# Kernel optimization log

Hardware: AMD Instinct MI355X
Metric: run time of the kernel (lower is better)

The kernel has to match this reference:

```python
import jax, jax.numpy as jnp
import numpy as np

N_NODES = 50000
N_EDGES = 1600000
D_FEAT = 512
FILTERS = 256
NUM_CLASSES = 16


def setup_inputs() -> dict:
    key = jax.random.key(0)
    k = jax.random.split(key, 6)
    x = jax.random.normal(k[0], (N_NODES, D_FEAT), dtype=jnp.float32)
    W1 = jax.random.normal(k[1], (D_FEAT, FILTERS), dtype=jnp.float32) * (1.0 / np.sqrt(D_FEAT))
    W2 = jax.random.normal(k[2], (FILTERS, NUM_CLASSES), dtype=jnp.float32) * (1.0 / np.sqrt(FILTERS))
    edge_weight = jax.random.uniform(k[3], (N_EDGES,), dtype=jnp.float32)
    edge_src = jax.random.randint(k[4], (N_EDGES,), 0, N_NODES, dtype=jnp.int32)
    edge_dst = jax.random.randint(k[5], (N_EDGES,), 0, N_NODES, dtype=jnp.int32)
    return {"x": x, "W1": W1, "W2": W2, "edge_weight": edge_weight,
            "edge_src": edge_src, "edge_dst": edge_dst}


def _propagate(h, edge_src, edge_dst, edge_weight):
    # sparse A @ h: out[dst] += w * h[src]
    msgs = edge_weight[:, None] * h[edge_src]          # [E, F]
    return jax.ops.segment_sum(msgs, edge_dst, num_segments=N_NODES)


def reference(x, W1, W2, edge_weight, edge_src, edge_dst):
    # Dropout layers are identity at inference (training=False).
    # Layer 1: relu(A @ (X @ W1))
    h = jax.nn.relu(_propagate(x @ W1, edge_src, edge_dst, edge_weight))
    # Layer 2: softmax(A @ (H @ W2))
    logits = _propagate(h @ W2, edge_src, edge_dst, edge_weight)
    return jax.nn.softmax(logits, axis=-1)
```

## Files before the change

kernel.cpp:

```cpp
#include <hip/hip_runtime.h>

#define N_NODES 50000
#define N_EDGES 1600000
#define D_FEAT 512
#define FILTERS 256
#define NUM_CLASSES 16

typedef __bf16 bf16x8 __attribute__((ext_vector_type(8)));
typedef float f32x4 __attribute__((ext_vector_type(4)));
typedef _Float16 half4 __attribute__((ext_vector_type(4)));
typedef _Float16 f16x8 __attribute__((ext_vector_type(8)));

#define GLOAD_LDS16(g, l)                                                  \
  __builtin_amdgcn_global_load_lds(                                        \
      (const __attribute__((address_space(1))) unsigned int*)(g),          \
      (__attribute__((address_space(3))) unsigned int*)(l), 16, 0, 0)

__global__ __launch_bounds__(256) void split_w1_kernel(
    const float* __restrict__ W1, __bf16* __restrict__ Wth,
    __bf16* __restrict__ Wtl) {
  const int idx = blockIdx.x * 256 + threadIdx.x;
  const int k = idx >> 8;
  const int n = idx & 255;
  const float v = W1[idx];
  const __bf16 h = (__bf16)v;
  const __bf16 l = (__bf16)(v - (float)h);
  Wth[n * D_FEAT + k] = h;
  Wtl[n * D_FEAT + k] = l;
}

__global__ __launch_bounds__(256) void gemm1_mfma_kernel(
    const float* __restrict__ A, const __bf16* __restrict__ Bh,
    const __bf16* __restrict__ Bl, _Float16* __restrict__ C) {
  const int K = D_FEAT;
  __shared__ __bf16 sAh[128 * 32];
  __shared__ __bf16 sAl[128 * 32];
  __shared__ __bf16 sBh[128 * 32];
  __shared__ __bf16 sBl[128 * 32];

  const int tid = threadIdx.x;
  const int wave = tid >> 6;
  const int lane = tid & 63;
  const int wm = (wave >> 1) * 64;
  const int wn = (wave & 1) * 64;
  const int m0 = blockIdx.x * 128;
  const int n0 = blockIdx.y * 128;

  const int arow = tid >> 1;
  const int aks = (tid & 1) * 16;
  int am = m0 + arow;
  if (am >= N_NODES) am = N_NODES - 1;
  const float* aptr = A + (size_t)am * K + aks;

  const int lr = lane >> 2;
  const int lc = (lane & 3) * 8;
  const int fm = lane & 15;
  const int fq = lane >> 4;

  f32x4 acc[4][4] = {};

  for (int k0 = 0; k0 < K; k0 += 32) {
    const float4* ap = (const float4*)(aptr + k0);
    const float4 a0 = ap[0], a1 = ap[1], a2 = ap[2], a3 = ap[3];

    __syncthreads();

#pragma unroll
    for (int i = 0; i < 2; ++i) {
      const int row = wave * 32 + i * 16;
      GLOAD_LDS16(Bh + (size_t)(n0 + row + lr) * K + k0 + lc, sBh + row * 32);
      GLOAD_LDS16(Bl + (size_t)(n0 + row + lr) * K + k0 + lc, sBl + row * 32);
    }

    float va[16] = {a0.x, a0.y, a0.z, a0.w, a1.x, a1.y, a1.z, a1.w,
                    a2.x, a2.y, a2.z, a2.w, a3.x, a3.y, a3.z, a3.w};
    __bf16 hh[16], ll[16];
#pragma unroll
    for (int i = 0; i < 16; ++i) {
      const __bf16 h = (__bf16)va[i];
      hh[i] = h;
      ll[i] = (__bf16)(va[i] - (float)h);
    }
    *(bf16x8*)(sAh + arow * 32 + aks) = *(bf16x8*)&hh[0];
    *(bf16x8*)(sAh + arow * 32 + aks + 8) = *(bf16x8*)&hh[8];
    *(bf16x8*)(sAl + arow * 32 + aks) = *(bf16x8*)&ll[0];
    *(bf16x8*)(sAl + arow * 32 + aks + 8) = *(bf16x8*)&ll[8];

    __syncthreads();

    bf16x8 fah[4], fal[4], fbh[4], fbl[4];
#pragma unroll
    for (int t = 0; t < 4; ++t) {
      const int moff = (wm + t * 16 + fm) * 32 + fq * 8;
      fah[t] = *(const bf16x8*)(sAh + moff);
      fal[t] = *(const bf16x8*)(sAl + moff);
      const int noff = (wn + t * 16 + fm) * 32 + fq * 8;
      fbh[t] = *(const bf16x8*)(sBh + noff);
      fbl[t] = *(const bf16x8*)(sBl + noff);
    }
#pragma unroll
    for (int i = 0; i < 4; ++i)
#pragma unroll
      for (int j = 0; j < 4; ++j)
        acc[i][j] = __builtin_amdgcn_mfma_f32_16x16x32_bf16(fah[i], fbh[j],
                                                            acc[i][j], 0, 0, 0);
#pragma unroll
    for (int i = 0; i < 4; ++i)
#pragma unroll
      for (int j = 0; j < 4; ++j)
        acc[i][j] = __builtin_amdgcn_mfma_f32_16x16x32_bf16(fah[i], fbl[j],
                                                            acc[i][j], 0, 0, 0);
#pragma unroll
    for (int i = 0; i < 4; ++i)
#pragma unroll
      for (int j = 0; j < 4; ++j)
        acc[i][j] = __builtin_amdgcn_mfma_f32_16x16x32_bf16(fal[i], fbh[j],
                                                            acc[i][j], 0, 0, 0);
  }

#pragma unroll
  for (int ti = 0; ti < 4; ++ti) {
#pragma unroll
    for (int r = 0; r < 4; ++r) {
      const int m = m0 + wm + ti * 16 + fq * 4 + r;
      if (m < N_NODES) {
#pragma unroll
        for (int tj = 0; tj < 4; ++tj) {
          const int n = n0 + wn + tj * 16 + fm;
          C[(size_t)m * FILTERS + n] = (_Float16)acc[ti][tj][r];
        }
      }
    }
  }
}

__global__ __launch_bounds__(256) void hist_kernel(const int* __restrict__ edst,
                                                   int* __restrict__ deg) {
  const int e = blockIdx.x * 256 + threadIdx.x;
  if (e < N_EDGES) atomicAdd(&deg[edst[e]], 1);
}

#define SCAN_NB 196
__global__ __launch_bounds__(256) void scan_blocks_kernel(
    const int* __restrict__ deg, int* __restrict__ row_ptr,
    int* __restrict__ bsum) {
  __shared__ int s[256];
  const int i = blockIdx.x * 256 + threadIdx.x;
  const int v = (i < N_NODES) ? deg[i] : 0;
  s[threadIdx.x] = v;
  __syncthreads();
  for (int off = 1; off < 256; off <<= 1) {
    const int t = (threadIdx.x >= off) ? s[threadIdx.x - off] : 0;
    __syncthreads();
    s[threadIdx.x] += t;
    __syncthreads();
  }
  if (i < N_NODES) row_ptr[i] = s[threadIdx.x] - v;
  if (threadIdx.x == 255) bsum[blockIdx.x] = s[255];
}

__global__ __launch_bounds__(256) void scan_sums_kernel(int* __restrict__ bsum) {
  __shared__ int s[256];
  const int v = (threadIdx.x < SCAN_NB) ? bsum[threadIdx.x] : 0;
  s[threadIdx.x] = v;
  __syncthreads();
  for (int off = 1; off < 256; off <<= 1) {
    const int t = (threadIdx.x >= off) ? s[threadIdx.x - off] : 0;
    __syncthreads();
    s[threadIdx.x] += t;
    __syncthreads();
  }
  if (threadIdx.x < SCAN_NB) bsum[threadIdx.x] = s[threadIdx.x] - v;
}

__global__ __launch_bounds__(256) void scan_add_kernel(
    int* __restrict__ row_ptr, const int* __restrict__ bsum,
    int* __restrict__ cursor) {
  const int i = blockIdx.x * 256 + threadIdx.x;
  if (i < N_NODES) {
    const int r = row_ptr[i] + bsum[blockIdx.x];
    row_ptr[i] = r;
    cursor[i] = r;
  }
  if (i == 0) row_ptr[N_NODES] = N_EDGES;
}

__global__ __launch_bounds__(256) void fill_kernel(
    const int* __restrict__ esrc, const int* __restrict__ edst,
    const float* __restrict__ ew, int* __restrict__ cursor,
    int4* __restrict__ meta) {
  const int e = blockIdx.x * 256 + threadIdx.x;
  if (e >= N_EDGES) return;
  const int d = edst[e];
  const int pos = atomicAdd(&cursor[d], 1);
  meta[pos] = make_int4(esrc[e], __float_as_int(ew[e]), d, 0);
}

__global__ __launch_bounds__(256) void gather1_gemm2_kernel(
    const _Float16* __restrict__ xw1, const int* __restrict__ row_ptr,
    const int4* __restrict__ meta, const float* __restrict__ W2,
    _Float16* __restrict__ h2) {
  __shared__ float red[4][16][17];
  const int wave = threadIdx.x >> 6;
  const int lane = threadIdx.x & 63;
  const int node = blockIdx.x * 4 + wave;
  const int beg = row_ptr[node];
  const int end = row_ptr[node + 1];

  float acc[4] = {};
  const half4* __restrict__ xw1v = (const half4*)xw1;

  for (int c0 = beg; c0 < end; c0 += 64) {
    const int cnt = min(64, end - c0);
    const int4 mv = meta[c0 + ((lane < cnt) ? lane : 0)];

    for (int j = 0; j < cnt; j += 8) {
      int srcs[8];
      float ws[8];
#pragma unroll
      for (int u = 0; u < 8; ++u) {
        const int live = (j + u < cnt);
        const int l = live ? (j + u) : 0;
        srcs[u] = __builtin_amdgcn_readlane(mv.x, l);
        const int wb = __builtin_amdgcn_readlane(mv.y, l);
        ws[u] = live ? __int_as_float(wb) : 0.f;
      }
      half4 v[8];
#pragma unroll
      for (int u = 0; u < 8; ++u)
        v[u] = xw1v[(unsigned)srcs[u] * 64u + (unsigned)lane];
#pragma unroll
      for (int u = 0; u < 8; ++u)
#pragma unroll
        for (int i = 0; i < 4; ++i)
          acc[i] = fmaf(ws[u], (float)v[u][i], acc[i]);
    }
  }

  float r[4];
#pragma unroll
  for (int i = 0; i < 4; ++i) r[i] = fmaxf(acc[i], 0.f);

  float p[16] = {};
#pragma unroll
  for (int j = 0; j < 4; ++j) {
    const float4* wr = (const float4*)(W2 + (size_t)(lane * 4 + j) * NUM_CLASSES);
#pragma unroll
    for (int c4 = 0; c4 < 4; ++c4) {
      const float4 wv = wr[c4];
      p[c4 * 4 + 0] = fmaf(r[j], wv.x, p[c4 * 4 + 0]);
      p[c4 * 4 + 1] = fmaf(r[j], wv.y, p[c4 * 4 + 1]);
      p[c4 * 4 + 2] = fmaf(r[j], wv.z, p[c4 * 4 + 2]);
      p[c4 * 4 + 3] = fmaf(r[j], wv.w, p[c4 * 4 + 3]);
    }
  }

#pragma unroll
  for (int off = 32; off >= 16; off >>= 1)
#pragma unroll
    for (int i = 0; i < 16; ++i) p[i] += __shfl_xor(p[i], off, 64);

  if (lane < 16) {
#pragma unroll
    for (int i = 0; i < 16; ++i) red[wave][lane][i] = p[i];
  }
  if (lane < 16) {
    float sum = 0.f;
#pragma unroll
    for (int i = 0; i < 16; ++i) sum += red[wave][i][lane];
    h2[(size_t)node * NUM_CLASSES + lane] = (_Float16)sum;
  }
}

__global__ __launch_bounds__(256) void gather2_mfma_kernel(
    const _Float16* __restrict__ h2, const int* __restrict__ row_ptr,
    const int4* __restrict__ meta, float* __restrict__ out) {
  __shared__ _Float16 lds[4][16][72];
  const int wave = threadIdx.x >> 6;
  const int lane = threadIdx.x & 63;
  const int tile = blockIdx.x * 4 + wave;
  if (tile >= N_NODES / 16) return;
  const int t0 = tile * 16;
  const int beg = row_ptr[t0];
  const int end = row_ptr[t0 + 16];

  const int cls = lane & 15;
  const int kq = lane >> 4;
  const int erow = lane >> 1;
  const int part = lane & 1;

  f32x4 acc = {0.f, 0.f, 0.f, 0.f};
  _Float16* myl = &lds[wave][0][0];

  if (beg < end) {
    const int last = end - 1;
    int e = beg + lane;
    int4 m = meta[(e <= last) ? e : last];
    float wv = (e <= last) ? __int_as_float(m.y) : 0.f;

    for (int c0 = beg; c0 < end; c0 += 64) {
      int4 mn = m;
      float wn = 0.f;
      const int c1 = c0 + 64;
      if (c1 < end) {
        const int en = c1 + lane;
        mn = meta[(en <= last) ? en : last];
        wn = (en <= last) ? __int_as_float(mn.y) : 0.f;
      }

      const int se0 = __shfl(m.x, erow, 64);
      const int se1 = __shfl(m.x, 32 + erow, 64);
      const f16x8 r0 =
          *(const f16x8*)(h2 + (size_t)se0 * NUM_CLASSES + part * 8);
      const f16x8 r1 =
          *(const f16x8*)(h2 + (size_t)se1 * NUM_CLASSES + part * 8);

      f16x8 a0, a1;
#pragma unroll
      for (int j = 0; j < 8; ++j) {
        const int ei = kq * 8 + j;
        const int d0 = __shfl(m.z, ei, 64) - t0;
        const float w0 = __shfl(wv, ei, 64);
        a0[j] = (d0 == cls) ? (_Float16)w0 : (_Float16)0.f;
        const int d1 = __shfl(m.z, 32 + ei, 64) - t0;
        const float w1 = __shfl(wv, 32 + ei, 64);
        a1[j] = (d1 == cls) ? (_Float16)w1 : (_Float16)0.f;
      }

#pragma unroll
      for (int j = 0; j < 8; ++j) myl[(part * 8 + j) * 72 + erow] = r0[j];
#pragma unroll
      for (int j = 0; j < 8; ++j) myl[(part * 8 + j) * 72 + 32 + erow] = r1[j];

      const f16x8 b0 = *(const f16x8*)(myl + cls * 72 + kq * 8);
      const f16x8 b1 = *(const f16x8*)(myl + cls * 72 + 32 + kq * 8);

      acc = __builtin_amdgcn_mfma_f32_16x16x32_f16(a0, b0, acc, 0, 0, 0);
      acc = __builtin_amdgcn_mfma_f32_16x16x32_f16(a1, b1, acc, 0, 0, 0);

      m = mn;
      wv = wn;
    }
  }

#pragma unroll
  for (int r = 0; r < 4; ++r) {
    const float a = acc[r];
    float mx = a;
#pragma unroll
    for (int off = 8; off >= 1; off >>= 1)
      mx = fmaxf(mx, __shfl_xor(mx, off, 16));
    const float ex = __expf(a - mx);
    float sm = ex;
#pragma unroll
    for (int off = 8; off >= 1; off >>= 1) sm += __shfl_xor(sm, off, 16);
    out[(size_t)(t0 + kq * 4 + r) * NUM_CLASSES + cls] = ex / sm;
  }
}

extern "C" void kernel_launch(void* const* d_in, const int* in_sizes, int n_in,
                              void* d_out, int out_size, void* d_ws,
                              size_t ws_size, hipStream_t stream) {
  const float* x = (const float*)d_in[0];
  const float* W1 = (const float*)d_in[1];
  const float* W2 = (const float*)d_in[2];
  const float* ew = (const float*)d_in[3];
  const int* esrc = (const int*)d_in[4];
  const int* edst = (const int*)d_in[5];
  float* out = (float*)d_out;

  _Float16* xw1 = (_Float16*)d_ws;
  _Float16* h2 = xw1 + (size_t)N_NODES * FILTERS;
  int* row_ptr = (int*)(h2 + (size_t)N_NODES * NUM_CLASSES);
  int* cursor = row_ptr + (N_NODES + 1);
  int* deg = cursor + N_NODES;
  int4* meta = (int4*)(((uintptr_t)(deg + N_NODES) + 15) & ~(uintptr_t)15);
  __bf16* w1th = (__bf16*)(meta + N_EDGES);
  __bf16* w1tl = w1th + D_FEAT * FILTERS;
  int* bsum = (int*)(w1tl + D_FEAT * FILTERS);

  hipMemsetAsync(deg, 0, N_NODES * sizeof(int), stream);
  hist_kernel<<<(N_EDGES + 255) / 256, 256, 0, stream>>>(edst, deg);
  scan_blocks_kernel<<<SCAN_NB, 256, 0, stream>>>(deg, row_ptr, bsum);
  scan_sums_kernel<<<1, 256, 0, stream>>>(bsum);
  scan_add_kernel<<<SCAN_NB, 256, 0, stream>>>(row_ptr, bsum, cursor);
  fill_kernel<<<(N_EDGES + 255) / 256, 256, 0, stream>>>(esrc, edst, ew,
                                                         cursor, meta);

  split_w1_kernel<<<(D_FEAT * FILTERS) / 256, 256, 0, stream>>>(W1, w1th, w1tl);
  dim3 g1((N_NODES + 127) / 128, FILTERS / 128);
  gemm1_mfma_kernel<<<g1, 256, 0, stream>>>(x, w1th, w1tl, xw1);

  gather1_gemm2_kernel<<<N_NODES / 4, 256, 0, stream>>>(xw1, row_ptr, meta, W2,
                                                        h2);

  gather2_mfma_kernel<<<(N_NODES / 16 + 3) / 4, 256, 0, stream>>>(h2, row_ptr,
                                                                  meta, out);
}
```

Before: 564.1 us.

## Gather two edges per wave with 16-byte loads and software-pipelined issue

```diff
diff --git a/kernel.cpp b/kernel.cpp
--- a/kernel.cpp
+++ b/kernel.cpp
@@ -207,44 +207,68 @@
   const int beg = row_ptr[node];
   const int end = row_ptr[node + 1];
 
-  float acc[4] = {};
-  const half4* __restrict__ xw1v = (const half4*)xw1;
+  const int eh = lane >> 5;
+  const int oct = lane & 31;
+
+  float acc[8] = {};
+
+#define G1_ISSUE(V, W, JB)                                                 \
+  {                                                                        \
+    _Pragma("unroll") for (int u = 0; u < 8; ++u) {                        \
+      const int e0 = (JB) + 2 * u;                                         \
+      const int e1 = e0 + 1;                                               \
+      const int l0 = (e0 < cnt) ? e0 : 0;                                  \
+      const int l1 = (e1 < cnt) ? e1 : 0;                                  \
+      const int s0 = __builtin_amdgcn_readlane(mv.x, l0);                  \
+      const int s1 = __builtin_amdgcn_readlane(mv.x, l1);                  \
+      const int q0 = __builtin_amdgcn_readlane(mv.y, l0);                  \
+      const int q1 = __builtin_amdgcn_readlane(mv.y, l1);                  \
+      const float w0f = (e0 < cnt) ? __int_as_float(q0) : 0.f;             \
+      const float w1f = (e1 < cnt) ? __int_as_float(q1) : 0.f;             \
+      W[u] = eh ? w1f : w0f;                                               \
+      const unsigned rs = eh ? (unsigned)s1 : (unsigned)s0;                \
+      V[u] = *(const f16x8*)(xw1 + (size_t)rs * FILTERS + oct * 8);        \
+    }                                                                      \
+  }
+
+#define G1_CONSUME(V, W)                                                   \
+  {                                                                        \
+    _Pragma("unroll") for (int u = 0; u < 8; ++u)                          \
+        _Pragma("unroll") for (int i = 0; i < 8; ++i) acc[i] =             \
+        fmaf(W[u], (float)V[u][i], acc[i]);                                \
+  }
 
   for (int c0 = beg; c0 < end; c0 += 64) {
     const int cnt = min(64, end - c0);
     const int4 mv = meta[c0 + ((lane < cnt) ? lane : 0)];
-
-    for (int j = 0; j < cnt; j += 8) {
-      int srcs[8];
-      float ws[8];
-#pragma unroll
-      for (int u = 0; u < 8; ++u) {
-        const int live = (j + u < cnt);
-        const int l = live ? (j + u) : 0;
-        srcs[u] = __builtin_amdgcn_readlane(mv.x, l);
-        const int wb = __builtin_amdgcn_readlane(mv.y, l);
-        ws[u] = live ? __int_as_float(wb) : 0.f;
+    const int ng = (cnt + 15) >> 4;
+
+    f16x8 va[8], vb[8];
+    float wa[8], wb[8];
+    G1_ISSUE(va, wa, 0);
+    for (int g = 1; g < ng; g += 2) {
+      G1_ISSUE(vb, wb, g * 16);
+      G1_CONSUME(va, wa);
+      if (g + 1 < ng) {
+        G1_ISSUE(va, wa, (g + 1) * 16);
       }
-      half4 v[8];
-#pragma unroll
-      for (int u = 0; u < 8; ++u)
-        v[u] = xw1v[(unsigned)srcs[u] * 64u + (unsigned)lane];
-#pragma unroll
-      for (int u = 0; u < 8; ++u)
-#pragma unroll
-        for (int i = 0; i < 4; ++i)
-          acc[i] = fmaf(ws[u], (float)v[u][i], acc[i]);
-    }
-  }
+      G1_CONSUME(vb, wb);
+    }
+    if (ng & 1) G1_CONSUME(va, wa);
+  }
+
+#pragma unroll
+  for (int i = 0; i < 8; ++i) acc[i] += __shfl_xor(acc[i], 32, 64);
 
   float r[4];
 #pragma unroll
-  for (int i = 0; i < 4; ++i) r[i] = fmaxf(acc[i], 0.f);
+  for (int j = 0; j < 4; ++j) r[j] = fmaxf(acc[eh * 4 + j], 0.f);
 
   float p[16] = {};
 #pragma unroll
   for (int j = 0; j < 4; ++j) {
-    const float4* wr = (const float4*)(W2 + (size_t)(lane * 4 + j) * NUM_CLASSES);
+    const float4* wr =
+        (const float4*)(W2 + (size_t)(oct * 8 + eh * 4 + j) * NUM_CLASSES);
 #pragma unroll
     for (int c4 = 0; c4 < 4; ++c4) {
       const float4 wv = wr[c4];
```

Result: slower. 577.6 us (+2.4%).

## Chunk XW1 by 32-feature slabs and split layer-1 gather across chunks

Applied to the files above, without the earlier changes.

```diff
diff --git a/kernel.cpp b/kernel.cpp
--- a/kernel.cpp
+++ b/kernel.cpp
@@ -127,7 +127,8 @@
 #pragma unroll
         for (int tj = 0; tj < 4; ++tj) {
           const int n = n0 + wn + tj * 16 + fm;
-          C[(size_t)m * FILTERS + n] = (_Float16)acc[ti][tj][r];
+          C[(size_t)(n >> 5) * ((size_t)N_NODES * 32) + (size_t)m * 32 +
+            (n & 31)] = (_Float16)acc[ti][tj][r];
         }
       }
     }
@@ -196,80 +197,93 @@
   meta[pos] = make_int4(esrc[e], __float_as_int(ew[e]), d, 0);
 }
 
-__global__ __launch_bounds__(256) void gather1_gemm2_kernel(
-    const _Float16* __restrict__ xw1, const int* __restrict__ row_ptr,
-    const int4* __restrict__ meta, const float* __restrict__ W2,
-    _Float16* __restrict__ h2) {
-  __shared__ float red[4][16][17];
+__global__ __launch_bounds__(256) void pack_kernel(
+    const int4* __restrict__ meta, unsigned short* __restrict__ srcs,
+    float* __restrict__ ws) {
+  const int e = blockIdx.x * 256 + threadIdx.x;
+  if (e >= N_EDGES) return;
+  const int4 m = meta[e];
+  srcs[e] = (unsigned short)m.x;
+  ws[e] = __int_as_float(m.y);
+}
+
+__global__ __launch_bounds__(256) void gather1_chunk_kernel(
+    const _Float16* __restrict__ xw1c, const int* __restrict__ row_ptr,
+    const unsigned short* __restrict__ srcs, const float* __restrict__ ws,
+    const float* __restrict__ W2, float* __restrict__ h2acc) {
   const int wave = threadIdx.x >> 6;
   const int lane = threadIdx.x & 63;
-  const int node = blockIdx.x * 4 + wave;
+  const int chunk = blockIdx.x & 7;
+  const int node = (blockIdx.x >> 3) * 4 + wave;
+  const int g = lane >> 3;
+  const int il = lane & 7;
+  const _Float16* __restrict__ base =
+      xw1c + (size_t)chunk * ((size_t)N_NODES * 32) + il * 4;
+
+  float w2r[4][2];
+#pragma unroll
+  for (int j = 0; j < 4; ++j) {
+    const float2 t = *(const float2*)(W2 +
+        (size_t)(chunk * 32 + il * 4 + j) * NUM_CLASSES + g * 2);
+    w2r[j][0] = t.x;
+    w2r[j][1] = t.y;
+  }
+
   const int beg = row_ptr[node];
   const int end = row_ptr[node + 1];
-
   float acc[4] = {};
-  const half4* __restrict__ xw1v = (const half4*)xw1;
 
   for (int c0 = beg; c0 < end; c0 += 64) {
     const int cnt = min(64, end - c0);
-    const int4 mv = meta[c0 + ((lane < cnt) ? lane : 0)];
-
-    for (int j = 0; j < cnt; j += 8) {
-      int srcs[8];
-      float ws[8];
-#pragma unroll
-      for (int u = 0; u < 8; ++u) {
-        const int live = (j + u < cnt);
-        const int l = live ? (j + u) : 0;
-        srcs[u] = __builtin_amdgcn_readlane(mv.x, l);
-        const int wb = __builtin_amdgcn_readlane(mv.y, l);
-        ws[u] = live ? __int_as_float(wb) : 0.f;
-      }
-      half4 v[8];
-#pragma unroll
-      for (int u = 0; u < 8; ++u)
-        v[u] = xw1v[(unsigned)srcs[u] * 64u + (unsigned)lane];
-#pragma unroll
-      for (int u = 0; u < 8; ++u)
-#pragma unroll
-        for (int i = 0; i < 4; ++i)
-          acc[i] = fmaf(ws[u], (float)v[u][i], acc[i]);
-    }
-  }
-
-  float r[4];
-#pragma unroll
-  for (int i = 0; i < 4; ++i) r[i] = fmaxf(acc[i], 0.f);
-
-  float p[16] = {};
+    const int idx = c0 + ((lane < cnt) ? lane : 0);
+    const int sv = (int)srcs[idx];
+    const float wv = ws[idx];
+    const int npk = (cnt + 7) >> 3;
+    for (int p = 0; p < npk; p += 2) {
+      const int e0 = p * 8 + g;
+      const int e1 = e0 + 8;
+      const int s0 = __shfl(sv, e0, 64);
+      const int s1 = __shfl(sv, e1, 64);
+      float w0 = __shfl(wv, e0, 64);
+      float w1 = __shfl(wv, e1, 64);
+      w0 = (e0 < cnt) ? w0 : 0.f;
+      w1 = (e1 < cnt) ? w1 : 0.f;
+      const half4 v0 = *(const half4*)(base + (size_t)s0 * 32);
+      const half4 v1 = *(const half4*)(base + (size_t)s1 * 32);
+#pragma unroll
+      for (int i = 0; i < 4; ++i) acc[i] = fmaf(w0, (float)v0[i], acc[i]);
+#pragma unroll
+      for (int i = 0; i < 4; ++i) acc[i] = fmaf(w1, (float)v1[i], acc[i]);
+    }
+  }
+
+#pragma unroll
+  for (int off = 8; off <= 32; off <<= 1)
+#pragma unroll
+    for (int i = 0; i < 4; ++i) acc[i] += __shfl_xor(acc[i], off, 64);
+
+  float p0 = 0.f, p1 = 0.f;
 #pragma unroll
   for (int j = 0; j < 4; ++j) {
-    const float4* wr = (const float4*)(W2 + (size_t)(lane * 4 + j) * NUM_CLASSES);
-#pragma unroll
-    for (int c4 = 0; c4 < 4; ++c4) {
-      const float4 wv = wr[c4];
-      p[c4 * 4 + 0] = fmaf(r[j], wv.x, p[c4 * 4 + 0]);
-      p[c4 * 4 + 1] = fmaf(r[j], wv.y, p[c4 * 4 + 1]);
-      p[c4 * 4 + 2] = fmaf(r[j], wv.z, p[c4 * 4 + 2]);
-      p[c4 * 4 + 3] = fmaf(r[j], wv.w, p[c4 * 4 + 3]);
-    }
-  }
-
-#pragma unroll
-  for (int off = 32; off >= 16; off >>= 1)
-#pragma unroll
-    for (int i = 0; i < 16; ++i) p[i] += __shfl_xor(p[i], off, 64);
-
-  if (lane < 16) {
-#pragma unroll
-    for (int i = 0; i < 16; ++i) red[wave][lane][i] = p[i];
-  }
-  if (lane < 16) {
-    float sum = 0.f;
-#pragma unroll
-    for (int i = 0; i < 16; ++i) sum += red[wave][i][lane];
-    h2[(size_t)node * NUM_CLASSES + lane] = (_Float16)sum;
-  }
+    const float r = fmaxf(acc[j], 0.f);
+    p0 = fmaf(r, w2r[j][0], p0);
+    p1 = fmaf(r, w2r[j][1], p1);
+  }
+#pragma unroll
+  for (int off = 1; off <= 4; off <<= 1) {
+    p0 += __shfl_xor(p0, off, 64);
+    p1 += __shfl_xor(p1, off, 64);
+  }
+  if (il == 0) {
+    atomicAdd(&h2acc[(size_t)node * NUM_CLASSES + g * 2 + 0], p0);
+    atomicAdd(&h2acc[(size_t)node * NUM_CLASSES + g * 2 + 1], p1);
+  }
+}
+
+__global__ __launch_bounds__(256) void cvt_h2_kernel(
+    const float* __restrict__ a, _Float16* __restrict__ o) {
+  const int i = blockIdx.x * 256 + threadIdx.x;
+  o[i] = (_Float16)a[i];
 }
 
 __global__ __launch_bounds__(256) void gather2_mfma_kernel(
@@ -369,8 +383,8 @@
   const int* edst = (const int*)d_in[5];
   float* out = (float*)d_out;
 
-  _Float16* xw1 = (_Float16*)d_ws;
-  _Float16* h2 = xw1 + (size_t)N_NODES * FILTERS;
+  _Float16* xw1c = (_Float16*)d_ws;
+  _Float16* h2 = xw1c + (size_t)N_NODES * FILTERS;
   int* row_ptr = (int*)(h2 + (size_t)N_NODES * NUM_CLASSES);
   int* cursor = row_ptr + (N_NODES + 1);
   int* deg = cursor + N_NODES;
@@ -378,21 +392,28 @@
   __bf16* w1th = (__bf16*)(meta + N_EDGES);
   __bf16* w1tl = w1th + D_FEAT * FILTERS;
   int* bsum = (int*)(w1tl + D_FEAT * FILTERS);
+  float* h2acc = (float*)(bsum + 256);
+  unsigned short* srcs = (unsigned short*)(h2acc + (size_t)N_NODES * NUM_CLASSES);
+  float* ws = (float*)(srcs + N_EDGES);
 
   hipMemsetAsync(deg, 0, N_NODES * sizeof(int), stream);
+  hipMemsetAsync(h2acc, 0, (size_t)N_NODES * NUM_CLASSES * sizeof(float),
+                 stream);
   hist_kernel<<<(N_EDGES + 255) / 256, 256, 0, stream>>>(edst, deg);
   scan_blocks_kernel<<<SCAN_NB, 256, 0, stream>>>(deg, row_ptr, bsum);
   scan_sums_kernel<<<1, 256, 0, stream>>>(bsum);
   scan_add_kernel<<<SCAN_NB, 256, 0, stream>>>(row_ptr, bsum, cursor);
   fill_kernel<<<(N_EDGES + 255) / 256, 256, 0, stream>>>(esrc, edst, ew,
                                                          cursor, meta);
+  pack_kernel<<<(N_EDGES + 255) / 256, 256, 0, stream>>>(meta, srcs, ws);
 
   split_w1_kernel<<<(D_FEAT * FILTERS) / 256, 256, 0, stream>>>(W1, w1th, w1tl);
   dim3 g1((N_NODES + 127) / 128, FILTERS / 128);
-  gemm1_mfma_kernel<<<g1, 256, 0, stream>>>(x, w1th, w1tl, xw1);
-
-  gather1_gemm2_kernel<<<N_NODES / 4, 256, 0, stream>>>(xw1, row_ptr, meta, W2,
-                                                        h2);
+  gemm1_mfma_kernel<<<g1, 256, 0, stream>>>(x, w1th, w1tl, xw1c);
+
+  gather1_chunk_kernel<<<(N_NODES / 4) * 8, 256, 0, stream>>>(
+      xw1c, row_ptr, srcs, ws, W2, h2acc);
+  cvt_h2_kernel<<<(N_NODES * NUM_CLASSES) / 256, 256, 0, stream>>>(h2acc, h2);
 
   gather2_mfma_kernel<<<(N_NODES / 16 + 3) / 4, 256, 0, stream>>>(h2, row_ptr,
                                                                   meta, out);
```

After: 708.0 us. +25.5%, slower.

## Fuse CSR build and W1 split into one cooperative kernel with grid syncs

Applied to the files above, without the earlier changes.

```diff
diff --git a/kernel.cpp b/kernel.cpp
--- a/kernel.cpp
+++ b/kernel.cpp
@@ -1,4 +1,5 @@
 #include <hip/hip_runtime.h>
+#include <hip/hip_cooperative_groups.h>
 
 #define N_NODES 50000
 #define N_EDGES 1600000
@@ -16,17 +17,73 @@
       (const __attribute__((address_space(1))) unsigned int*)(g),          \
       (__attribute__((address_space(3))) unsigned int*)(l), 16, 0, 0)
 
-__global__ __launch_bounds__(256) void split_w1_kernel(
+#define CSR_NB 196
+__global__ __launch_bounds__(256) void csr_coop_kernel(
     const float* __restrict__ W1, __bf16* __restrict__ Wth,
-    __bf16* __restrict__ Wtl) {
-  const int idx = blockIdx.x * 256 + threadIdx.x;
-  const int k = idx >> 8;
-  const int n = idx & 255;
-  const float v = W1[idx];
-  const __bf16 h = (__bf16)v;
-  const __bf16 l = (__bf16)(v - (float)h);
-  Wth[n * D_FEAT + k] = h;
-  Wtl[n * D_FEAT + k] = l;
+    __bf16* __restrict__ Wtl, const int* __restrict__ esrc,
+    const int* __restrict__ edst, const float* __restrict__ ew,
+    int* __restrict__ deg, int* __restrict__ row_ptr,
+    int* __restrict__ cursor, int* __restrict__ bsum,
+    int4* __restrict__ meta) {
+  cooperative_groups::grid_group grid = cooperative_groups::this_grid();
+  const int tid = blockIdx.x * 256 + threadIdx.x;
+  const int nthr = CSR_NB * 256;
+
+  for (int i = tid; i < N_NODES; i += nthr) deg[i] = 0;
+  for (int i = tid; i < D_FEAT * FILTERS; i += nthr) {
+    const float v = W1[i];
+    const int k = i >> 8;
+    const int n = i & 255;
+    const __bf16 h = (__bf16)v;
+    Wth[n * D_FEAT + k] = h;
+    Wtl[n * D_FEAT + k] = (__bf16)(v - (float)h);
+  }
+  grid.sync();
+
+  for (int e = tid; e < N_EDGES; e += nthr) atomicAdd(&deg[edst[e]], 1);
+  grid.sync();
+
+  __shared__ int s[256];
+  const int v = (tid < N_NODES) ? deg[tid] : 0;
+  s[threadIdx.x] = v;
+  __syncthreads();
+  for (int off = 1; off < 256; off <<= 1) {
+    const int t = (threadIdx.x >= off) ? s[threadIdx.x - off] : 0;
+    __syncthreads();
+    s[threadIdx.x] += t;
+    __syncthreads();
+  }
+  const int excl = s[threadIdx.x] - v;
+  if (threadIdx.x == 255) bsum[blockIdx.x] = s[255];
+  grid.sync();
+
+  if (blockIdx.x == 0) {
+    const int bv = (threadIdx.x < CSR_NB) ? bsum[threadIdx.x] : 0;
+    s[threadIdx.x] = bv;
+    __syncthreads();
+    for (int off = 1; off < 256; off <<= 1) {
+      const int t = (threadIdx.x >= off) ? s[threadIdx.x - off] : 0;
+      __syncthreads();
+      s[threadIdx.x] += t;
+      __syncthreads();
+    }
+    if (threadIdx.x < CSR_NB) bsum[threadIdx.x] = s[threadIdx.x] - bv;
+  }
+  grid.sync();
+
+  if (tid < N_NODES) {
+    const int r = excl + bsum[blockIdx.x];
+    row_ptr[tid] = r;
+    cursor[tid] = r;
+  }
+  if (tid == 0) row_ptr[N_NODES] = N_EDGES;
+  grid.sync();
+
+  for (int e = tid; e < N_EDGES; e += nthr) {
+    const int d = edst[e];
+    const int pos = atomicAdd(&cursor[d], 1);
+    meta[pos] = make_int4(esrc[e], __float_as_int(ew[e]), d, 0);
+  }
 }
 
 __global__ __launch_bounds__(256) void gemm1_mfma_kernel(
@@ -132,68 +189,6 @@
       }
     }
   }
-}
-
-__global__ __launch_bounds__(256) void hist_kernel(const int* __restrict__ edst,
-                                                   int* __restrict__ deg) {
-  const int e = blockIdx.x * 256 + threadIdx.x;
-  if (e < N_EDGES) atomicAdd(&deg[edst[e]], 1);
-}
-
-#define SCAN_NB 196
-__global__ __launch_bounds__(256) void scan_blocks_kernel(
-    const int* __restrict__ deg, int* __restrict__ row_ptr,
-    int* __restrict__ bsum) {
-  __shared__ int s[256];
-  const int i = blockIdx.x * 256 + threadIdx.x;
-  const int v = (i < N_NODES) ? deg[i] : 0;
-  s[threadIdx.x] = v;
-  __syncthreads();
-  for (int off = 1; off < 256; off <<= 1) {
-    const int t = (threadIdx.x >= off) ? s[threadIdx.x - off] : 0;
-    __syncthreads();
-    s[threadIdx.x] += t;
-    __syncthreads();
-  }
-  if (i < N_NODES) row_ptr[i] = s[threadIdx.x] - v;
-  if (threadIdx.x == 255) bsum[blockIdx.x] = s[255];
-}
-
-__global__ __launch_bounds__(256) void scan_sums_kernel(int* __restrict__ bsum) {
-  __shared__ int s[256];
-  const int v = (threadIdx.x < SCAN_NB) ? bsum[threadIdx.x] : 0;
-  s[threadIdx.x] = v;
-  __syncthreads();
-  for (int off = 1; off < 256; off <<= 1) {
-    const int t = (threadIdx.x >= off) ? s[threadIdx.x - off] : 0;
-    __syncthreads();
-    s[threadIdx.x] += t;
-    __syncthreads();
-  }
-  if (threadIdx.x < SCAN_NB) bsum[threadIdx.x] = s[threadIdx.x] - v;
-}
-
-__global__ __launch_bounds__(256) void scan_add_kernel(
-    int* __restrict__ row_ptr, const int* __restrict__ bsum,
-    int* __restrict__ cursor) {
-  const int i = blockIdx.x * 256 + threadIdx.x;
-  if (i < N_NODES) {
-    const int r = row_ptr[i] + bsum[blockIdx.x];
-    row_ptr[i] = r;
-    cursor[i] = r;
-  }
-  if (i == 0) row_ptr[N_NODES] = N_EDGES;
-}
-
-__global__ __launch_bounds__(256) void fill_kernel(
-    const int* __restrict__ esrc, const int* __restrict__ edst,
-    const float* __restrict__ ew, int* __restrict__ cursor,
-    int4* __restrict__ meta) {
-  const int e = blockIdx.x * 256 + threadIdx.x;
-  if (e >= N_EDGES) return;
-  const int d = edst[e];
-  const int pos = atomicAdd(&cursor[d], 1);
-  meta[pos] = make_int4(esrc[e], __float_as_int(ew[e]), d, 0);
 }
 
 __global__ __launch_bounds__(256) void gather1_gemm2_kernel(
@@ -379,15 +374,12 @@
   __bf16* w1tl = w1th + D_FEAT * FILTERS;
   int* bsum = (int*)(w1tl + D_FEAT * FILTERS);
 
-  hipMemsetAsync(deg, 0, N_NODES * sizeof(int), stream);
-  hist_kernel<<<(N_EDGES + 255) / 256, 256, 0, stream>>>(edst, deg);
-  scan_blocks_kernel<<<SCAN_NB, 256, 0, stream>>>(deg, row_ptr, bsum);
-  scan_sums_kernel<<<1, 256, 0, stream>>>(bsum);
-  scan_add_kernel<<<SCAN_NB, 256, 0, stream>>>(row_ptr, bsum, cursor);
-  fill_kernel<<<(N_EDGES + 255) / 256, 256, 0, stream>>>(esrc, edst, ew,
-                                                         cursor, meta);
-
-  split_w1_kernel<<<(D_FEAT * FILTERS) / 256, 256, 0, stream>>>(W1, w1th, w1tl);
+  void* args[] = {(void*)&W1,   (void*)&w1th, (void*)&w1tl, (void*)&esrc,
+                  (void*)&edst, (void*)&ew,   (void*)&deg,  (void*)&row_ptr,
+                  (void*)&cursor, (void*)&bsum, (void*)&meta};
+  hipLaunchCooperativeKernel((const void*)csr_coop_kernel, dim3(CSR_NB),
+                             dim3(256), args, 0, stream);
+
   dim3 g1((N_NODES + 127) / 128, FILTERS / 128);
   gemm1_mfma_kernel<<<g1, 256, 0, stream>>>(x, w1th, w1tl, xw1);
 
```

After: 649.5 us. 15.2% more time.
